# Kernel tuning notes

Hardware: AMD Instinct MI355X
Metric: run time of the kernel (lower is better)

The kernel has to match this reference:

```python
import jax, jax.numpy as jnp
import numpy as np

N, E, F_IN, H, G, C = 50000, 600000, 128, 128, 500, 10


def _lin(k, fi, fo):
    # Glorot-ish scaled init for a [fi, fo] weight
    return (jax.random.normal(k, (fi, fo), jnp.float32) / np.float32(np.sqrt(fi)))


def setup_inputs() -> dict:
    key = jax.random.key(0)
    ks = jax.random.split(key, 16)
    x = jax.random.normal(ks[0], (N, F_IN), jnp.float32)
    edge_index = jax.random.randint(ks[1], (2, E), 0, N, dtype=jnp.int32)
    batch = jnp.sort(jax.random.randint(ks[2], (N,), 0, G, dtype=jnp.int32))
    return {
        "x": x, "edge_index": edge_index, "batch": batch,
        # SAGEConv i: out = mean_aggr @ Wl + bl + x @ Wr  (PyG default: mean aggr, root weight, bias on lin_l)
        "Wl1": _lin(ks[3], F_IN, H), "bl1": jnp.zeros((H,), jnp.float32), "Wr1": _lin(ks[4], F_IN, H),
        "Wl2": _lin(ks[5], H, H),    "bl2": jnp.zeros((H,), jnp.float32), "Wr2": _lin(ks[6], H, H),
        "Wl3": _lin(ks[7], H, H),    "bl3": jnp.zeros((H,), jnp.float32), "Wr3": _lin(ks[8], H, H),
        "W4": _lin(ks[9], H, 64), "b4": jnp.zeros((64,), jnp.float32),
        "W5": _lin(ks[10], 64, C), "b5": jnp.zeros((C,), jnp.float32),
    }


def _segment_mean(vals, ids, num_segments):
    s = jax.ops.segment_sum(vals, ids, num_segments=num_segments)
    cnt = jax.ops.segment_sum(jnp.ones((vals.shape[0], 1), vals.dtype), ids, num_segments=num_segments)
    return s / jnp.maximum(cnt, 1.0)


def _sage_conv(x, src, dst, Wl, bl, Wr):
    # gather source features along edges, mean-aggregate at destinations
    aggr = _segment_mean(x[src], dst, N)  # [N, F]
    return aggr @ Wl + bl + x @ Wr


def reference(x, edge_index, batch, Wl1, bl1, Wr1, Wl2, bl2, Wr2, Wl3, bl3, Wr3, W4, b4, W5, b5):
    src, dst = edge_index[0], edge_index[1]
    h = jax.nn.relu(_sage_conv(x, src, dst, Wl1, bl1, Wr1))
    h = jax.nn.relu(_sage_conv(h, src, dst, Wl2, bl2, Wr2))
    h = jax.nn.relu(_sage_conv(h, src, dst, Wl3, bl3, Wr3))
    g = _segment_mean(h, batch, G)          # global mean pool -> [G, H]
    g = jax.nn.relu(g @ W4 + b4)
    return jax.nn.log_softmax(g @ W5 + b5, axis=-1)
```

## Files before the change

### kernel.cpp

```cpp
#include <hip/hip_runtime.h>
#include <hip/hip_bf16.h>
#include <math.h>

#define FH 128

typedef __attribute__((ext_vector_type(8))) short short8v;
typedef __attribute__((ext_vector_type(4))) float float4v;
typedef unsigned short ushort_t;
typedef unsigned int   uint32;

__device__ __forceinline__ ushort_t f2bf(float f) {
    uint32 u = __builtin_bit_cast(uint32, f);
    u += 0x7fffu + ((u >> 16) & 1u);
    return (ushort_t)(u >> 16);
}
__device__ __forceinline__ float bf_lo(uint32 w) { return __builtin_bit_cast(float, w << 16); }
__device__ __forceinline__ float bf_hi(uint32 w) { return __builtin_bit_cast(float, w & 0xffff0000u); }
__device__ __forceinline__ uint32 pack2(float lo, float hi) {
    return (uint32)f2bf(lo) | ((uint32)f2bf(hi) << 16);
}

__device__ __forceinline__ void pack_one(const float* __restrict__ Wl,
                                         const float* __restrict__ Wr,
                                         ushort_t* __restrict__ Bp, int t) {
    int k = t >> 7, n = t & 127;
    float v = (k < FH) ? Wl[k * FH + n] : Wr[(k - FH) * FH + n];
    int nt = n >> 4, kt = k >> 5;
    int lane = (n & 15) + (((k >> 3) & 3) << 4);
    int j = k & 7;
    Bp[(((nt * 8 + kt) * 64) + lane) * 8 + j] = f2bf(v);
}

__global__ __launch_bounds__(256) void prep_kernel(
        const float* __restrict__ x, ushort_t* __restrict__ xb, size_t n, int cvtBlocks,
        const float* __restrict__ Wl1, const float* __restrict__ Wr1, ushort_t* __restrict__ Bp1,
        const float* __restrict__ Wl2, const float* __restrict__ Wr2, ushort_t* __restrict__ Bp2,
        const float* __restrict__ Wl3, const float* __restrict__ Wr3, ushort_t* __restrict__ Bp3,
        int* __restrict__ deg, int N) {
    int b = blockIdx.x;
    if (b < cvtBlocks) {
        size_t base = ((size_t)b * 256 + threadIdx.x) * 8;
        if (base >= n) return;
        const float4 a = *(const float4*)(x + base);
        const float4 c = *(const float4*)(x + base + 4);
        ushort_t o[8] = {f2bf(a.x), f2bf(a.y), f2bf(a.z), f2bf(a.w),
                         f2bf(c.x), f2bf(c.y), f2bf(c.z), f2bf(c.w)};
        *(uint4*)(xb + base) = *(const uint4*)o;
        return;
    }
    b -= cvtBlocks;
    if (b < 384) {
        int which = b >> 7;
        int t = (b & 127) * 256 + threadIdx.x;
        if (which == 0)      pack_one(Wl1, Wr1, Bp1, t);
        else if (which == 1) pack_one(Wl2, Wr2, Bp2, t);
        else                 pack_one(Wl3, Wr3, Bp3, t);
        return;
    }
    b -= 384;
    {
        int i = (b * 256 + threadIdx.x) * 4;
        if (i + 3 < N) {
            *(int4*)(deg + i) = make_int4(0, 0, 0, 0);
        } else {
            for (int j = i; j < N; ++j) deg[j] = 0;
        }
    }
}

__global__ __launch_bounds__(256) void deg_kernel(const int* __restrict__ dst,
                                                  int* __restrict__ deg, int E) {
    int e = blockIdx.x * 256 + threadIdx.x;
    if (e < E) atomicAdd(&deg[dst[e]], 1);
}

__global__ __launch_bounds__(256) void scan1_kernel(const int* __restrict__ deg,
                                                    int* __restrict__ rowptr,
                                                    int* __restrict__ blockSums, int N) {
    __shared__ int lds[256];
    const int base = blockIdx.x * 1024;
    const int t = threadIdx.x;
    int v[4]; int sum = 0;
    #pragma unroll
    for (int j = 0; j < 4; ++j) {
        int idx = base + t * 4 + j;
        v[j] = (idx < N) ? deg[idx] : 0;
        sum += v[j];
    }
    lds[t] = sum; __syncthreads();
    for (int off = 1; off < 256; off <<= 1) {
        int val = lds[t];
        int add = (t >= off) ? lds[t - off] : 0;
        __syncthreads();
        lds[t] = val + add;
        __syncthreads();
    }
    int run = (t > 0) ? lds[t - 1] : 0;
    #pragma unroll
    for (int j = 0; j < 4; ++j) {
        int idx = base + t * 4 + j;
        if (idx < N) rowptr[idx] = run;
        run += v[j];
    }
    if (t == 255) blockSums[blockIdx.x] = lds[255];
}

__global__ __launch_bounds__(256) void scan3_gb_kernel(int* __restrict__ rowptr,
                                                       int* __restrict__ pos,
                                                       const int* __restrict__ blockSums,
                                                       int N, int nb,
                                                       const int* __restrict__ batch,
                                                       int* __restrict__ gstart, int G) {
    if ((int)blockIdx.x >= nb) {
        int g = ((int)blockIdx.x - nb) * 256 + threadIdx.x;
        if (g > G) return;
        int lo = 0, hi = N;
        while (lo < hi) {
            int mid = (lo + hi) >> 1;
            if (batch[mid] < g) lo = mid + 1; else hi = mid;
        }
        gstart[g] = lo;
        return;
    }
    __shared__ int sAdd, sTot;
    if (threadIdx.x < 64) {
        const int lane = threadIdx.x;
        const int bid = blockIdx.x;
        int pre = 0, tot = 0;
        for (int i = lane; i < nb; i += 64) {
            const int v = blockSums[i];
            tot += v;
            if (i < bid) pre += v;
        }
        #pragma unroll
        for (int off = 1; off < 64; off <<= 1) {
            pre += __shfl_xor(pre, off);
            tot += __shfl_xor(tot, off);
        }
        if (lane == 0) { sAdd = pre; sTot = tot; }
    }
    __syncthreads();
    const int add = sAdd;
    const int base = blockIdx.x * 1024;
    #pragma unroll
    for (int j = 0; j < 4; ++j) {
        int idx = base + threadIdx.x * 4 + j;
        if (idx < N) {
            int v = rowptr[idx] + add;
            rowptr[idx] = v;
            pos[idx] = v;
        }
    }
    if (blockIdx.x == (unsigned)(nb - 1) && threadIdx.x == 0) rowptr[N] = sTot;
}

__global__ __launch_bounds__(256) void fill_csr_kernel(const int* __restrict__ src,
                                                       const int* __restrict__ dst,
                                                       int* __restrict__ pos,
                                                       int* __restrict__ csr, int E) {
    int e = (blockIdx.x * 256 + threadIdx.x) * 2;
    if (e >= E) return;
    if (e + 1 < E) {
        const int2 s2 = *(const int2*)(src + e);
        const int2 d2 = *(const int2*)(dst + e);
        int i0 = atomicAdd(&pos[d2.x], 1);
        int i1 = atomicAdd(&pos[d2.y], 1);
        csr[i0] = s2.x;
        csr[i1] = s2.y;
    } else {
        int idx = atomicAdd(&pos[dst[e]], 1);
        csr[idx] = src[e];
    }
}

__global__ __launch_bounds__(256) void pull_mean_kernel(const ushort_t* __restrict__ x,
                                                        const int* __restrict__ rowptr,
                                                        const int* __restrict__ csr,
                                                        ushort_t* __restrict__ aggr, int N) {
    const int v = (blockIdx.x * 256 + threadIdx.x) >> 6;
    if (v >= N) return;
    const int lane = threadIdx.x & 63;
    const int grp  = lane >> 4;
    const int li   = lane & 15;
    const int beg = rowptr[v], end = rowptr[v + 1];
    const uint4* xp = (const uint4*)x + li;

    const uint4 z = {0u, 0u, 0u, 0u};
    uint4 w0 = z, w1 = z, w2 = z, w3 = z, w4 = z, w5 = z;
    const int i0 = beg + grp;
    if (i0 < end)      w0 = xp[(size_t)csr[i0] * 16];
    if (i0 + 4 < end)  w1 = xp[(size_t)csr[i0 + 4] * 16];
    if (i0 + 8 < end)  w2 = xp[(size_t)csr[i0 + 8] * 16];
    if (i0 + 12 < end) w3 = xp[(size_t)csr[i0 + 12] * 16];
    if (i0 + 16 < end) w4 = xp[(size_t)csr[i0 + 16] * 16];
    if (i0 + 20 < end) w5 = xp[(size_t)csr[i0 + 20] * 16];

    float a0 = (bf_lo(w0.x) + bf_lo(w1.x)) + (bf_lo(w2.x) + bf_lo(w3.x)) + (bf_lo(w4.x) + bf_lo(w5.x));
    float a1 = (bf_hi(w0.x) + bf_hi(w1.x)) + (bf_hi(w2.x) + bf_hi(w3.x)) + (bf_hi(w4.x) + bf_hi(w5.x));
    float a2 = (bf_lo(w0.y) + bf_lo(w1.y)) + (bf_lo(w2.y) + bf_lo(w3.y)) + (bf_lo(w4.y) + bf_lo(w5.y));
    float a3 = (bf_hi(w0.y) + bf_hi(w1.y)) + (bf_hi(w2.y) + bf_hi(w3.y)) + (bf_hi(w4.y) + bf_hi(w5.y));
    float a4 = (bf_lo(w0.z) + bf_lo(w1.z)) + (bf_lo(w2.z) + bf_lo(w3.z)) + (bf_lo(w4.z) + bf_lo(w5.z));
    float a5 = (bf_hi(w0.z) + bf_hi(w1.z)) + (bf_hi(w2.z) + bf_hi(w3.z)) + (bf_hi(w4.z) + bf_hi(w5.z));
    float a6 = (bf_lo(w0.w) + bf_lo(w1.w)) + (bf_lo(w2.w) + bf_lo(w3.w)) + (bf_lo(w4.w) + bf_lo(w5.w));
    float a7 = (bf_hi(w0.w) + bf_hi(w1.w)) + (bf_hi(w2.w) + bf_hi(w3.w)) + (bf_hi(w4.w) + bf_hi(w5.w));

    for (int i = beg + 24 + grp; i < end; i += 4) {
        const uint4 w = xp[(size_t)csr[i] * 16];
        a0 += bf_lo(w.x); a1 += bf_hi(w.x); a2 += bf_lo(w.y); a3 += bf_hi(w.y);
        a4 += bf_lo(w.z); a5 += bf_hi(w.z); a6 += bf_lo(w.w); a7 += bf_hi(w.w);
    }

    a0 += __shfl_xor(a0, 16); a1 += __shfl_xor(a1, 16);
    a2 += __shfl_xor(a2, 16); a3 += __shfl_xor(a3, 16);
    a4 += __shfl_xor(a4, 16); a5 += __shfl_xor(a5, 16);
    a6 += __shfl_xor(a6, 16); a7 += __shfl_xor(a7, 16);
    a0 += __shfl_xor(a0, 32); a1 += __shfl_xor(a1, 32);
    a2 += __shfl_xor(a2, 32); a3 += __shfl_xor(a3, 32);
    a4 += __shfl_xor(a4, 32); a5 += __shfl_xor(a5, 32);
    a6 += __shfl_xor(a6, 32); a7 += __shfl_xor(a7, 32);

    if (grp == 0) {
        const float inv = 1.0f / (float)max(end - beg, 1);
        uint4 o;
        o.x = pack2(a0 * inv, a1 * inv);
        o.y = pack2(a2 * inv, a3 * inv);
        o.z = pack2(a4 * inv, a5 * inv);
        o.w = pack2(a6 * inv, a7 * inv);
        ((uint4*)aggr)[(size_t)v * 16 + li] = o;
    }
}

#define SO_STRIDE 136
__global__ __launch_bounds__(512) void sage_mfma_kernel(const ushort_t* __restrict__ xin,
                                                        const ushort_t* __restrict__ aggr,
                                                        const ushort_t* __restrict__ Bp,
                                                        const float* __restrict__ bl,
                                                        ushort_t* __restrict__ out, int M) {
    __shared__ ushort_t sB[32768];
    const int tid = threadIdx.x;
    {
        const uint4* s = (const uint4*)Bp;
        uint4* d = (uint4*)sB;
        #pragma unroll
        for (int i = 0; i < 8; ++i)
            d[tid + 512 * i] = s[tid + 512 * i];
    }
    __syncthreads();

    const int wave = tid >> 6;
    const int lane = tid & 63;
    const int grp  = lane >> 4;
    const int li   = lane & 15;
    const int rowBase = (blockIdx.x * 8 + wave) * 16;
    const int arow = min(rowBase + li, M - 1);

    short8v afrag[8];
    #pragma unroll
    for (int kt = 0; kt < 4; ++kt)
        afrag[kt] = *(const short8v*)(aggr + (size_t)arow * FH + kt * 32 + grp * 8);
    #pragma unroll
    for (int kt = 0; kt < 4; ++kt)
        afrag[4 + kt] = *(const short8v*)(xin + (size_t)arow * FH + kt * 32 + grp * 8);

    float4v acc[8];
    #pragma unroll
    for (int nt = 0; nt < 8; ++nt) {
        acc[nt] = (float4v){0.f, 0.f, 0.f, 0.f};
        #pragma unroll
        for (int kt = 0; kt < 8; ++kt) {
            const short8v b = *(const short8v*)(sB + (((nt * 8 + kt) * 64) + lane) * 8);
            acc[nt] = __builtin_amdgcn_mfma_f32_16x16x32_bf16(afrag[kt], b, acc[nt], 0, 0, 0);
        }
    }

    __syncthreads();

    ushort_t* so = sB + wave * (16 * SO_STRIDE);
    #pragma unroll
    for (int nt = 0; nt < 8; ++nt) {
        const float bias = bl[nt * 16 + li];
        #pragma unroll
        for (int r = 0; r < 4; ++r)
            so[(grp * 4 + r) * SO_STRIDE + nt * 16 + li] = f2bf(fmaxf(acc[nt][r] + bias, 0.f));
    }
    #pragma unroll
    for (int t = 0; t < 4; ++t) {
        const int idx = lane + 64 * t;
        const int r  = idx >> 4;
        const int ch = idx & 15;
        const int row = rowBase + r;
        if (row < M) {
            const uint4 val = *(const uint4*)(so + r * SO_STRIDE + ch * 8);
            *(uint4*)(out + (size_t)row * FH + ch * 8) = val;
        }
    }
}

__global__ __launch_bounds__(256) void head_kernel(const ushort_t* __restrict__ h,
                                                   const int* __restrict__ gstart,
                                                   const float* __restrict__ W4,
                                                   const float* __restrict__ b4,
                                                   const float* __restrict__ W5,
                                                   const float* __restrict__ b5,
                                                   float* __restrict__ out, int G) {
    __shared__ float sred[4][FH];
    __shared__ float sg2[64];
    __shared__ float sl[10];
    __shared__ float slse;
    const int g = blockIdx.x;
    const int t = threadIdx.x;
    const int wave = t >> 6, lane = t & 63;
    const int beg = gstart[g], end = gstart[g + 1];

    const uint32* hp = (const uint32*)h + lane;
    float a0 = 0.f, a1 = 0.f;
    for (int i = beg + wave; i < end; i += 4) {
        const uint32 w = hp[(size_t)i * 64];
        a0 += bf_lo(w); a1 += bf_hi(w);
    }
    sred[wave][lane * 2]     = a0;
    sred[wave][lane * 2 + 1] = a1;
    __syncthreads();
    if (t < FH) {
        const float s = sred[0][t] + sred[1][t] + sred[2][t] + sred[3][t];
        sred[0][t] = s / (float)max(end - beg, 1);
    }
    __syncthreads();
    if (t < 64) {
        float acc = b4[t];
        #pragma unroll 4
        for (int k = 0; k < FH; ++k)
            acc += sred[0][k] * W4[k * 64 + t];
        sg2[t] = fmaxf(acc, 0.f);
    }
    __syncthreads();
    if (t < 10) {
        float acc = b5[t];
        #pragma unroll 4
        for (int k = 0; k < 64; ++k)
            acc += sg2[k] * W5[k * 10 + t];
        sl[t] = acc;
    }
    __syncthreads();
    if (t == 0) {
        float m = sl[0];
        #pragma unroll
        for (int j = 1; j < 10; ++j) m = fmaxf(m, sl[j]);
        float s = 0.f;
        #pragma unroll
        for (int j = 0; j < 10; ++j) s += expf(sl[j] - m);
        slse = m + logf(s);
    }
    __syncthreads();
    if (t < 10) out[g * 10 + t] = sl[t] - slse;
}

extern "C" void kernel_launch(void* const* d_in, const int* in_sizes, int n_in,
                              void* d_out, int out_size, void* d_ws, size_t ws_size,
                              hipStream_t stream) {
    const float* x     = (const float*)d_in[0];
    const int*   ei    = (const int*)d_in[1];
    const int*   batch = (const int*)d_in[2];
    const float* Wl1 = (const float*)d_in[3];
    const float* bl1 = (const float*)d_in[4];
    const float* Wr1 = (const float*)d_in[5];
    const float* Wl2 = (const float*)d_in[6];
    const float* bl2 = (const float*)d_in[7];
    const float* Wr2 = (const float*)d_in[8];
    const float* Wl3 = (const float*)d_in[9];
    const float* bl3 = (const float*)d_in[10];
    const float* Wr3 = (const float*)d_in[11];
    const float* W4  = (const float*)d_in[12];
    const float* b4  = (const float*)d_in[13];
    const float* W5  = (const float*)d_in[14];
    const float* b5  = (const float*)d_in[15];
    float* out = (float*)d_out;

    const int N = in_sizes[0] / FH;
    const int E = in_sizes[1] / 2;
    const int G = out_size / 10;
    const int* src = ei;
    const int* dst = ei + E;

    char* p = (char*)d_ws;
    auto take = [&](size_t bytes) { char* q = p; p += (bytes + 255) & ~(size_t)255; return q; };
    ushort_t* xb    = (ushort_t*)take((size_t)N * FH * 2);
    ushort_t* h     = (ushort_t*)take((size_t)N * FH * 2);
    ushort_t* aggrb = (ushort_t*)take((size_t)N * FH * 2);
    int* deg        = (int*)take((size_t)N * 4);
    int* rowptr     = (int*)take((size_t)(N + 1) * 4);
    int* pos        = (int*)take((size_t)N * 4);
    int* csr        = (int*)take((size_t)E * 4);
    int* blockSums  = (int*)take(256 * 4);
    ushort_t* Bp1   = (ushort_t*)take(256 * FH * 2);
    ushort_t* Bp2   = (ushort_t*)take(256 * FH * 2);
    ushort_t* Bp3   = (ushort_t*)take(256 * FH * 2);
    int* gstart     = (int*)take((size_t)(G + 1) * 4);

    const int nb = (N + 1023) / 1024;

    const int cvtBlocks  = (int)(((size_t)N * FH / 8 + 255) / 256);
    const int zeroBlocks = (N / 4 + 255) / 256;
    prep_kernel<<<cvtBlocks + 384 + zeroBlocks, 256, 0, stream>>>(
        x, xb, (size_t)N * FH, cvtBlocks,
        Wl1, Wr1, Bp1, Wl2, Wr2, Bp2, Wl3, Wr3, Bp3,
        deg, N);

    deg_kernel<<<(E + 255) / 256, 256, 0, stream>>>(dst, deg, E);

    const int gbBlocks = (G + 1 + 255) / 256;
    scan1_kernel<<<nb, 256, 0, stream>>>(deg, rowptr, blockSums, N);
    scan3_gb_kernel<<<nb + gbBlocks, 256, 0, stream>>>(rowptr, pos, blockSums, N, nb,
                                                       batch, gstart, G);
    fill_csr_kernel<<<(E / 2 + 255) / 256, 256, 0, stream>>>(src, dst, pos, csr, E);

    const int pullGrid = (N * 64 + 255) / 256;
    const int gemmGrid = (N + 127) / 128;

    pull_mean_kernel<<<pullGrid, 256, 0, stream>>>(xb, rowptr, csr, aggrb, N);
    sage_mfma_kernel<<<gemmGrid, 512, 0, stream>>>(xb, aggrb, Bp1, bl1, h, N);

    pull_mean_kernel<<<pullGrid, 256, 0, stream>>>(h, rowptr, csr, aggrb, N);
    sage_mfma_kernel<<<gemmGrid, 512, 0, stream>>>(h, aggrb, Bp2, bl2, h, N);

    pull_mean_kernel<<<pullGrid, 256, 0, stream>>>(h, rowptr, csr, aggrb, N);
    sage_mfma_kernel<<<gemmGrid, 512, 0, stream>>>(h, aggrb, Bp3, bl3, h, N);

    head_kernel<<<G, 256, 0, stream>>>(h, gstart, W4, b4, W5, b5, out, G);
}
```

Baseline: 210.4 us.

## Fuse two-pass scan into single-pass lookback scan and use 16 lanes per node

Merges the two CSR prefix-scan kernels into one kernel that publishes each block's sum with an agent-scope flag; later blocks spin on earlier blocks' flags to get their prefix. The flags live just past the degree array, so prep_kernel now zeroes them too. The mean-aggregation gather now gives each node 16 lanes instead of 64, with 12 neighbour loads unrolled and no cross-lane shuffle reduction. This cuts one launch and the shuffle work, at the cost of spin-waiting that assumes earlier blocks get scheduled, and less parallelism per node for high-degree nodes.

Result: slower. 227.1 us (+8.0%).

```diff
diff --git a/kernel.cpp b/kernel.cpp
--- a/kernel.cpp
+++ b/kernel.cpp
@@ -36,7 +36,7 @@
         const float* __restrict__ Wl1, const float* __restrict__ Wr1, ushort_t* __restrict__ Bp1,
         const float* __restrict__ Wl2, const float* __restrict__ Wr2, ushort_t* __restrict__ Bp2,
         const float* __restrict__ Wl3, const float* __restrict__ Wr3, ushort_t* __restrict__ Bp3,
-        int* __restrict__ deg, int N) {
+        int* __restrict__ deg, int Nz) {
     int b = blockIdx.x;
     if (b < cvtBlocks) {
         size_t base = ((size_t)b * 256 + threadIdx.x) * 8;
@@ -60,10 +60,10 @@
     b -= 384;
     {
         int i = (b * 256 + threadIdx.x) * 4;
-        if (i + 3 < N) {
+        if (i + 3 < Nz) {
             *(int4*)(deg + i) = make_int4(0, 0, 0, 0);
         } else {
-            for (int j = i; j < N; ++j) deg[j] = 0;
+            for (int j = i; j < Nz; ++j) deg[j] = 0;
         }
     }
 }
@@ -74,43 +74,14 @@
     if (e < E) atomicAdd(&deg[dst[e]], 1);
 }
 
-__global__ __launch_bounds__(256) void scan1_kernel(const int* __restrict__ deg,
-                                                    int* __restrict__ rowptr,
-                                                    int* __restrict__ blockSums, int N) {
-    __shared__ int lds[256];
-    const int base = blockIdx.x * 1024;
-    const int t = threadIdx.x;
-    int v[4]; int sum = 0;
-    #pragma unroll
-    for (int j = 0; j < 4; ++j) {
-        int idx = base + t * 4 + j;
-        v[j] = (idx < N) ? deg[idx] : 0;
-        sum += v[j];
-    }
-    lds[t] = sum; __syncthreads();
-    for (int off = 1; off < 256; off <<= 1) {
-        int val = lds[t];
-        int add = (t >= off) ? lds[t - off] : 0;
-        __syncthreads();
-        lds[t] = val + add;
-        __syncthreads();
-    }
-    int run = (t > 0) ? lds[t - 1] : 0;
-    #pragma unroll
-    for (int j = 0; j < 4; ++j) {
-        int idx = base + t * 4 + j;
-        if (idx < N) rowptr[idx] = run;
-        run += v[j];
-    }
-    if (t == 255) blockSums[blockIdx.x] = lds[255];
-}
-
-__global__ __launch_bounds__(256) void scan3_gb_kernel(int* __restrict__ rowptr,
-                                                       int* __restrict__ pos,
-                                                       const int* __restrict__ blockSums,
-                                                       int N, int nb,
-                                                       const int* __restrict__ batch,
-                                                       int* __restrict__ gstart, int G) {
+__global__ __launch_bounds__(256) void scan_lb_kernel(const int* __restrict__ deg,
+                                                      int* __restrict__ rowptr,
+                                                      int* __restrict__ pos,
+                                                      int* __restrict__ lsum,
+                                                      int* __restrict__ lflag,
+                                                      int N, int nb,
+                                                      const int* __restrict__ batch,
+                                                      int* __restrict__ gstart, int G) {
     if ((int)blockIdx.x >= nb) {
         int g = ((int)blockIdx.x - nb) * 256 + threadIdx.x;
         if (g > G) return;
@@ -122,36 +93,53 @@
         gstart[g] = lo;
         return;
     }
-    __shared__ int sAdd, sTot;
-    if (threadIdx.x < 64) {
-        const int lane = threadIdx.x;
-        const int bid = blockIdx.x;
-        int pre = 0, tot = 0;
-        for (int i = lane; i < nb; i += 64) {
-            const int v = blockSums[i];
-            tot += v;
-            if (i < bid) pre += v;
+    __shared__ int lds[256];
+    __shared__ int sPre;
+    const int b = blockIdx.x;
+    const int base = b * 1024;
+    const int t = threadIdx.x;
+    int v[4]; int sum = 0;
+    #pragma unroll
+    for (int j = 0; j < 4; ++j) {
+        int idx = base + t * 4 + j;
+        v[j] = (idx < N) ? deg[idx] : 0;
+        sum += v[j];
+    }
+    lds[t] = sum; __syncthreads();
+    for (int off = 1; off < 256; off <<= 1) {
+        int val = lds[t];
+        int add = (t >= off) ? lds[t - off] : 0;
+        __syncthreads();
+        lds[t] = val + add;
+        __syncthreads();
+    }
+    if (t == 255) {
+        __hip_atomic_store(&lsum[b], lds[255], __ATOMIC_RELAXED, __HIP_MEMORY_SCOPE_AGENT);
+        __hip_atomic_store(&lflag[b], 1, __ATOMIC_RELEASE, __HIP_MEMORY_SCOPE_AGENT);
+    }
+    if (t < 64) {
+        int pre = 0;
+        if (t < b) {
+            while (__hip_atomic_load(&lflag[t], __ATOMIC_ACQUIRE, __HIP_MEMORY_SCOPE_AGENT) == 0) {}
+            pre = __hip_atomic_load(&lsum[t], __ATOMIC_RELAXED, __HIP_MEMORY_SCOPE_AGENT);
         }
         #pragma unroll
-        for (int off = 1; off < 64; off <<= 1) {
+        for (int off = 1; off < 64; off <<= 1)
             pre += __shfl_xor(pre, off);
-            tot += __shfl_xor(tot, off);
-        }
-        if (lane == 0) { sAdd = pre; sTot = tot; }
-    }
-    __syncthreads();
-    const int add = sAdd;
-    const int base = blockIdx.x * 1024;
+        if (t == 0) sPre = pre;
+    }
+    __syncthreads();
+    const int add = sPre;
+    int run = add + ((t > 0) ? lds[t - 1] : 0) - sum;
+    int ex = add + ((t > 0) ? lds[t - 1] : 0);
+    (void)run;
     #pragma unroll
     for (int j = 0; j < 4; ++j) {
-        int idx = base + threadIdx.x * 4 + j;
-        if (idx < N) {
-            int v = rowptr[idx] + add;
-            rowptr[idx] = v;
-            pos[idx] = v;
-        }
-    }
-    if (blockIdx.x == (unsigned)(nb - 1) && threadIdx.x == 0) rowptr[N] = sTot;
+        int idx = base + t * 4 + j;
+        if (idx < N) { rowptr[idx] = ex; pos[idx] = ex; }
+        ex += v[j];
+    }
+    if (b == nb - 1 && t == 255) rowptr[N] = add + lds[255];
 }
 
 __global__ __launch_bounds__(256) void fill_csr_kernel(const int* __restrict__ src,
@@ -177,57 +165,42 @@
                                                         const int* __restrict__ rowptr,
                                                         const int* __restrict__ csr,
                                                         ushort_t* __restrict__ aggr, int N) {
-    const int v = (blockIdx.x * 256 + threadIdx.x) >> 6;
-    if (v >= N) return;
-    const int lane = threadIdx.x & 63;
-    const int grp  = lane >> 4;
-    const int li   = lane & 15;
-    const int beg = rowptr[v], end = rowptr[v + 1];
+    const int node = (blockIdx.x * 256 + threadIdx.x) >> 4;
+    if (node >= N) return;
+    const int li = threadIdx.x & 15;
+    const int beg = rowptr[node], end = rowptr[node + 1];
     const uint4* xp = (const uint4*)x + li;
 
     const uint4 z = {0u, 0u, 0u, 0u};
-    uint4 w0 = z, w1 = z, w2 = z, w3 = z, w4 = z, w5 = z;
-    const int i0 = beg + grp;
-    if (i0 < end)      w0 = xp[(size_t)csr[i0] * 16];
-    if (i0 + 4 < end)  w1 = xp[(size_t)csr[i0 + 4] * 16];
-    if (i0 + 8 < end)  w2 = xp[(size_t)csr[i0 + 8] * 16];
-    if (i0 + 12 < end) w3 = xp[(size_t)csr[i0 + 12] * 16];
-    if (i0 + 16 < end) w4 = xp[(size_t)csr[i0 + 16] * 16];
-    if (i0 + 20 < end) w5 = xp[(size_t)csr[i0 + 20] * 16];
-
-    float a0 = (bf_lo(w0.x) + bf_lo(w1.x)) + (bf_lo(w2.x) + bf_lo(w3.x)) + (bf_lo(w4.x) + bf_lo(w5.x));
-    float a1 = (bf_hi(w0.x) + bf_hi(w1.x)) + (bf_hi(w2.x) + bf_hi(w3.x)) + (bf_hi(w4.x) + bf_hi(w5.x));
-    float a2 = (bf_lo(w0.y) + bf_lo(w1.y)) + (bf_lo(w2.y) + bf_lo(w3.y)) + (bf_lo(w4.y) + bf_lo(w5.y));
-    float a3 = (bf_hi(w0.y) + bf_hi(w1.y)) + (bf_hi(w2.y) + bf_hi(w3.y)) + (bf_hi(w4.y) + bf_hi(w5.y));
-    float a4 = (bf_lo(w0.z) + bf_lo(w1.z)) + (bf_lo(w2.z) + bf_lo(w3.z)) + (bf_lo(w4.z) + bf_lo(w5.z));
-    float a5 = (bf_hi(w0.z) + bf_hi(w1.z)) + (bf_hi(w2.z) + bf_hi(w3.z)) + (bf_hi(w4.z) + bf_hi(w5.z));
-    float a6 = (bf_lo(w0.w) + bf_lo(w1.w)) + (bf_lo(w2.w) + bf_lo(w3.w)) + (bf_lo(w4.w) + bf_lo(w5.w));
-    float a7 = (bf_hi(w0.w) + bf_hi(w1.w)) + (bf_hi(w2.w) + bf_hi(w3.w)) + (bf_hi(w4.w) + bf_hi(w5.w));
-
-    for (int i = beg + 24 + grp; i < end; i += 4) {
-        const uint4 w = xp[(size_t)csr[i] * 16];
-        a0 += bf_lo(w.x); a1 += bf_hi(w.x); a2 += bf_lo(w.y); a3 += bf_hi(w.y);
-        a4 += bf_lo(w.z); a5 += bf_hi(w.z); a6 += bf_lo(w.w); a7 += bf_hi(w.w);
-    }
-
-    a0 += __shfl_xor(a0, 16); a1 += __shfl_xor(a1, 16);
-    a2 += __shfl_xor(a2, 16); a3 += __shfl_xor(a3, 16);
-    a4 += __shfl_xor(a4, 16); a5 += __shfl_xor(a5, 16);
-    a6 += __shfl_xor(a6, 16); a7 += __shfl_xor(a7, 16);
-    a0 += __shfl_xor(a0, 32); a1 += __shfl_xor(a1, 32);
-    a2 += __shfl_xor(a2, 32); a3 += __shfl_xor(a3, 32);
-    a4 += __shfl_xor(a4, 32); a5 += __shfl_xor(a5, 32);
-    a6 += __shfl_xor(a6, 32); a7 += __shfl_xor(a7, 32);
-
-    if (grp == 0) {
-        const float inv = 1.0f / (float)max(end - beg, 1);
-        uint4 o;
-        o.x = pack2(a0 * inv, a1 * inv);
-        o.y = pack2(a2 * inv, a3 * inv);
-        o.z = pack2(a4 * inv, a5 * inv);
-        o.w = pack2(a6 * inv, a7 * inv);
-        ((uint4*)aggr)[(size_t)v * 16 + li] = o;
-    }
+    uint4 w[12];
+    #pragma unroll
+    for (int k = 0; k < 12; ++k)
+        w[k] = (beg + k < end) ? xp[(size_t)csr[beg + k] * 16] : z;
+
+    float a0 = 0.f, a1 = 0.f, a2 = 0.f, a3 = 0.f;
+    float a4 = 0.f, a5 = 0.f, a6 = 0.f, a7 = 0.f;
+    #pragma unroll
+    for (int k = 0; k < 12; ++k) {
+        a0 += bf_lo(w[k].x); a1 += bf_hi(w[k].x);
+        a2 += bf_lo(w[k].y); a3 += bf_hi(w[k].y);
+        a4 += bf_lo(w[k].z); a5 += bf_hi(w[k].z);
+        a6 += bf_lo(w[k].w); a7 += bf_hi(w[k].w);
+    }
+    for (int i = beg + 12; i < end; ++i) {
+        const uint4 ww = xp[(size_t)csr[i] * 16];
+        a0 += bf_lo(ww.x); a1 += bf_hi(ww.x);
+        a2 += bf_lo(ww.y); a3 += bf_hi(ww.y);
+        a4 += bf_lo(ww.z); a5 += bf_hi(ww.z);
+        a6 += bf_lo(ww.w); a7 += bf_hi(ww.w);
+    }
+
+    const float inv = 1.0f / (float)max(end - beg, 1);
+    uint4 o;
+    o.x = pack2(a0 * inv, a1 * inv);
+    o.y = pack2(a2 * inv, a3 * inv);
+    o.z = pack2(a4 * inv, a5 * inv);
+    o.w = pack2(a6 * inv, a7 * inv);
+    ((uint4*)aggr)[(size_t)node * 16 + li] = o;
 }
 
 #define SO_STRIDE 136
@@ -387,11 +360,12 @@
     ushort_t* xb    = (ushort_t*)take((size_t)N * FH * 2);
     ushort_t* h     = (ushort_t*)take((size_t)N * FH * 2);
     ushort_t* aggrb = (ushort_t*)take((size_t)N * FH * 2);
-    int* deg        = (int*)take((size_t)N * 4);
+    int* deg        = (int*)take((size_t)(N + 64) * 4);
+    int* lflag      = deg + N;
     int* rowptr     = (int*)take((size_t)(N + 1) * 4);
     int* pos        = (int*)take((size_t)N * 4);
     int* csr        = (int*)take((size_t)E * 4);
-    int* blockSums  = (int*)take(256 * 4);
+    int* lsum       = (int*)take(256 * 4);
     ushort_t* Bp1   = (ushort_t*)take(256 * FH * 2);
     ushort_t* Bp2   = (ushort_t*)take(256 * FH * 2);
     ushort_t* Bp3   = (ushort_t*)take(256 * FH * 2);
@@ -400,21 +374,20 @@
     const int nb = (N + 1023) / 1024;
 
     const int cvtBlocks  = (int)(((size_t)N * FH / 8 + 255) / 256);
-    const int zeroBlocks = (N / 4 + 255) / 256;
+    const int zeroBlocks = ((N + 64) / 4 + 255) / 256;
     prep_kernel<<<cvtBlocks + 384 + zeroBlocks, 256, 0, stream>>>(
         x, xb, (size_t)N * FH, cvtBlocks,
         Wl1, Wr1, Bp1, Wl2, Wr2, Bp2, Wl3, Wr3, Bp3,
-        deg, N);
+        deg, N + 64);
 
     deg_kernel<<<(E + 255) / 256, 256, 0, stream>>>(dst, deg, E);
 
     const int gbBlocks = (G + 1 + 255) / 256;
-    scan1_kernel<<<nb, 256, 0, stream>>>(deg, rowptr, blockSums, N);
-    scan3_gb_kernel<<<nb + gbBlocks, 256, 0, stream>>>(rowptr, pos, blockSums, N, nb,
-                                                       batch, gstart, G);
+    scan_lb_kernel<<<nb + gbBlocks, 256, 0, stream>>>(deg, rowptr, pos, lsum, lflag,
+                                                      N, nb, batch, gstart, G);
     fill_csr_kernel<<<(E / 2 + 255) / 256, 256, 0, stream>>>(src, dst, pos, csr, E);
 
-    const int pullGrid = (N * 64 + 255) / 256;
+    const int pullGrid = (N * 16 + 255) / 256;
     const int gemmGrid = (N + 127) / 128;
 
     pull_mean_kernel<<<pullGrid, 256, 0, stream>>>(xb, rowptr, csr, aggrb, N);
```

## Fuse CSR construction stages into one cooperative kernel with grid syncs

Applied to the files above, without the earlier changes.

The separate kernels for zeroing degrees, counting degrees, block scan, scan fixup plus graph-start search, and CSR fill become one cooperative kernel of 1024 blocks that separates the phases with grid-wide syncs. Degree zeroing moves out of the prep kernel into this kernel. The aim is to remove several kernel launches and their inter-kernel gaps. In exchange, the edge phases are limited to a fixed grid using grid-stride loops, and each grid.sync adds its own cost.

Measured after the change: 572.9 us. 2.72x slower.

```diff
diff --git a/kernel.cpp b/kernel.cpp
--- a/kernel.cpp
+++ b/kernel.cpp
@@ -1,5 +1,6 @@
 #include <hip/hip_runtime.h>
 #include <hip/hip_bf16.h>
+#include <hip/hip_cooperative_groups.h>
 #include <math.h>
 
 #define FH 128
@@ -35,8 +36,7 @@
         const float* __restrict__ x, ushort_t* __restrict__ xb, size_t n, int cvtBlocks,
         const float* __restrict__ Wl1, const float* __restrict__ Wr1, ushort_t* __restrict__ Bp1,
         const float* __restrict__ Wl2, const float* __restrict__ Wr2, ushort_t* __restrict__ Bp2,
-        const float* __restrict__ Wl3, const float* __restrict__ Wr3, ushort_t* __restrict__ Bp3,
-        int* __restrict__ deg, int N) {
+        const float* __restrict__ Wl3, const float* __restrict__ Wr3, ushort_t* __restrict__ Bp3) {
     int b = blockIdx.x;
     if (b < cvtBlocks) {
         size_t base = ((size_t)b * 256 + threadIdx.x) * 8;
@@ -49,127 +49,120 @@
         return;
     }
     b -= cvtBlocks;
-    if (b < 384) {
+    {
         int which = b >> 7;
         int t = (b & 127) * 256 + threadIdx.x;
         if (which == 0)      pack_one(Wl1, Wr1, Bp1, t);
         else if (which == 1) pack_one(Wl2, Wr2, Bp2, t);
         else                 pack_one(Wl3, Wr3, Bp3, t);
-        return;
-    }
-    b -= 384;
-    {
-        int i = (b * 256 + threadIdx.x) * 4;
-        if (i + 3 < N) {
-            *(int4*)(deg + i) = make_int4(0, 0, 0, 0);
+    }
+}
+
+__global__ __launch_bounds__(256) void csr_coop_kernel(const int* __restrict__ src,
+                                                       const int* __restrict__ dst,
+                                                       int* __restrict__ deg,
+                                                       int* __restrict__ rowptr,
+                                                       int* __restrict__ pos,
+                                                       int* __restrict__ csr,
+                                                       int* __restrict__ blockSums,
+                                                       const int* __restrict__ batch,
+                                                       int* __restrict__ gstart,
+                                                       int N, int E, int G, int nb) {
+    cooperative_groups::grid_group grid = cooperative_groups::this_grid();
+    const int t   = threadIdx.x;
+    const int bid = blockIdx.x;
+    const int nthr = gridDim.x * 256;
+    const int gtid = bid * 256 + t;
+
+    for (int i = gtid; i < N; i += nthr) deg[i] = 0;
+    grid.sync();
+
+    for (int e = gtid; e < E; e += nthr) atomicAdd(&deg[dst[e]], 1);
+    grid.sync();
+
+    if (bid < nb) {
+        __shared__ int lds[256];
+        const int base = bid * 1024;
+        int v[4]; int sum = 0;
+        #pragma unroll
+        for (int j = 0; j < 4; ++j) {
+            int idx = base + t * 4 + j;
+            v[j] = (idx < N) ? deg[idx] : 0;
+            sum += v[j];
+        }
+        lds[t] = sum; __syncthreads();
+        for (int off = 1; off < 256; off <<= 1) {
+            int val = lds[t];
+            int add = (t >= off) ? lds[t - off] : 0;
+            __syncthreads();
+            lds[t] = val + add;
+            __syncthreads();
+        }
+        int run = (t > 0) ? lds[t - 1] : 0;
+        #pragma unroll
+        for (int j = 0; j < 4; ++j) {
+            int idx = base + t * 4 + j;
+            if (idx < N) rowptr[idx] = run;
+            run += v[j];
+        }
+        if (t == 255) blockSums[bid] = lds[255];
+    } else if (bid < nb + 2) {
+        int g = (bid - nb) * 256 + t;
+        if (g <= G) {
+            int lo = 0, hi = N;
+            while (lo < hi) {
+                int mid = (lo + hi) >> 1;
+                if (batch[mid] < g) lo = mid + 1; else hi = mid;
+            }
+            gstart[g] = lo;
+        }
+    }
+    grid.sync();
+
+    if (bid < nb) {
+        __shared__ int sAdd, sTot;
+        if (t < 64) {
+            int pre = 0, tot = 0;
+            for (int i = t; i < nb; i += 64) {
+                const int v = blockSums[i];
+                tot += v;
+                if (i < bid) pre += v;
+            }
+            #pragma unroll
+            for (int off = 1; off < 64; off <<= 1) {
+                pre += __shfl_xor(pre, off);
+                tot += __shfl_xor(tot, off);
+            }
+            if (t == 0) { sAdd = pre; sTot = tot; }
+        }
+        __syncthreads();
+        const int add = sAdd;
+        const int base = bid * 1024;
+        #pragma unroll
+        for (int j = 0; j < 4; ++j) {
+            int idx = base + t * 4 + j;
+            if (idx < N) {
+                int v = rowptr[idx] + add;
+                rowptr[idx] = v;
+                pos[idx] = v;
+            }
+        }
+        if (bid == nb - 1 && t == 0) rowptr[N] = sTot;
+    }
+    grid.sync();
+
+    for (int e = gtid * 2; e < E; e += nthr * 2) {
+        if (e + 1 < E) {
+            const int2 s2 = *(const int2*)(src + e);
+            const int2 d2 = *(const int2*)(dst + e);
+            int i0 = atomicAdd(&pos[d2.x], 1);
+            int i1 = atomicAdd(&pos[d2.y], 1);
+            csr[i0] = s2.x;
+            csr[i1] = s2.y;
         } else {
-            for (int j = i; j < N; ++j) deg[j] = 0;
-        }
-    }
-}
-
-__global__ __launch_bounds__(256) void deg_kernel(const int* __restrict__ dst,
-                                                  int* __restrict__ deg, int E) {
-    int e = blockIdx.x * 256 + threadIdx.x;
-    if (e < E) atomicAdd(&deg[dst[e]], 1);
-}
-
-__global__ __launch_bounds__(256) void scan1_kernel(const int* __restrict__ deg,
-                                                    int* __restrict__ rowptr,
-                                                    int* __restrict__ blockSums, int N) {
-    __shared__ int lds[256];
-    const int base = blockIdx.x * 1024;
-    const int t = threadIdx.x;
-    int v[4]; int sum = 0;
-    #pragma unroll
-    for (int j = 0; j < 4; ++j) {
-        int idx = base + t * 4 + j;
-        v[j] = (idx < N) ? deg[idx] : 0;
-        sum += v[j];
-    }
-    lds[t] = sum; __syncthreads();
-    for (int off = 1; off < 256; off <<= 1) {
-        int val = lds[t];
-        int add = (t >= off) ? lds[t - off] : 0;
-        __syncthreads();
-        lds[t] = val + add;
-        __syncthreads();
-    }
-    int run = (t > 0) ? lds[t - 1] : 0;
-    #pragma unroll
-    for (int j = 0; j < 4; ++j) {
-        int idx = base + t * 4 + j;
-        if (idx < N) rowptr[idx] = run;
-        run += v[j];
-    }
-    if (t == 255) blockSums[blockIdx.x] = lds[255];
-}
-
-__global__ __launch_bounds__(256) void scan3_gb_kernel(int* __restrict__ rowptr,
-                                                       int* __restrict__ pos,
-                                                       const int* __restrict__ blockSums,
-                                                       int N, int nb,
-                                                       const int* __restrict__ batch,
-                                                       int* __restrict__ gstart, int G) {
-    if ((int)blockIdx.x >= nb) {
-        int g = ((int)blockIdx.x - nb) * 256 + threadIdx.x;
-        if (g > G) return;
-        int lo = 0, hi = N;
-        while (lo < hi) {
-            int mid = (lo + hi) >> 1;
-            if (batch[mid] < g) lo = mid + 1; else hi = mid;
-        }
-        gstart[g] = lo;
-        return;
-    }
-    __shared__ int sAdd, sTot;
-    if (threadIdx.x < 64) {
-        const int lane = threadIdx.x;
-        const int bid = blockIdx.x;
-        int pre = 0, tot = 0;
-        for (int i = lane; i < nb; i += 64) {
-            const int v = blockSums[i];
-            tot += v;
-            if (i < bid) pre += v;
-        }
-        #pragma unroll
-        for (int off = 1; off < 64; off <<= 1) {
-            pre += __shfl_xor(pre, off);
-            tot += __shfl_xor(tot, off);
-        }
-        if (lane == 0) { sAdd = pre; sTot = tot; }
-    }
-    __syncthreads();
-    const int add = sAdd;
-    const int base = blockIdx.x * 1024;
-    #pragma unroll
-    for (int j = 0; j < 4; ++j) {
-        int idx = base + threadIdx.x * 4 + j;
-        if (idx < N) {
-            int v = rowptr[idx] + add;
-            rowptr[idx] = v;
-            pos[idx] = v;
-        }
-    }
-    if (blockIdx.x == (unsigned)(nb - 1) && threadIdx.x == 0) rowptr[N] = sTot;
-}
-
-__global__ __launch_bounds__(256) void fill_csr_kernel(const int* __restrict__ src,
-                                                       const int* __restrict__ dst,
-                                                       int* __restrict__ pos,
-                                                       int* __restrict__ csr, int E) {
-    int e = (blockIdx.x * 256 + threadIdx.x) * 2;
-    if (e >= E) return;
-    if (e + 1 < E) {
-        const int2 s2 = *(const int2*)(src + e);
-        const int2 d2 = *(const int2*)(dst + e);
-        int i0 = atomicAdd(&pos[d2.x], 1);
-        int i1 = atomicAdd(&pos[d2.y], 1);
-        csr[i0] = s2.x;
-        csr[i1] = s2.y;
-    } else {
-        int idx = atomicAdd(&pos[dst[e]], 1);
-        csr[idx] = src[e];
+            int idx = atomicAdd(&pos[dst[e]], 1);
+            csr[idx] = src[e];
+        }
     }
 }
 
@@ -397,22 +390,23 @@
     ushort_t* Bp3   = (ushort_t*)take(256 * FH * 2);
     int* gstart     = (int*)take((size_t)(G + 1) * 4);
 
-    const int nb = (N + 1023) / 1024;
-
-    const int cvtBlocks  = (int)(((size_t)N * FH / 8 + 255) / 256);
-    const int zeroBlocks = (N / 4 + 255) / 256;
-    prep_kernel<<<cvtBlocks + 384 + zeroBlocks, 256, 0, stream>>>(
+    int nb = (N + 1023) / 1024;
+
+    const int cvtBlocks = (int)(((size_t)N * FH / 8 + 255) / 256);
+    prep_kernel<<<cvtBlocks + 384, 256, 0, stream>>>(
         x, xb, (size_t)N * FH, cvtBlocks,
-        Wl1, Wr1, Bp1, Wl2, Wr2, Bp2, Wl3, Wr3, Bp3,
-        deg, N);
-
-    deg_kernel<<<(E + 255) / 256, 256, 0, stream>>>(dst, deg, E);
-
-    const int gbBlocks = (G + 1 + 255) / 256;
-    scan1_kernel<<<nb, 256, 0, stream>>>(deg, rowptr, blockSums, N);
-    scan3_gb_kernel<<<nb + gbBlocks, 256, 0, stream>>>(rowptr, pos, blockSums, N, nb,
-                                                       batch, gstart, G);
-    fill_csr_kernel<<<(E / 2 + 255) / 256, 256, 0, stream>>>(src, dst, pos, csr, E);
+        Wl1, Wr1, Bp1, Wl2, Wr2, Bp2, Wl3, Wr3, Bp3);
+
+    {
+        int N_ = N, E_ = E, G_ = G, nb_ = nb;
+        const int* src_ = src; const int* dst_ = dst;
+        int* deg_ = deg; int* rowptr_ = rowptr; int* pos_ = pos; int* csr_ = csr;
+        int* bsum_ = blockSums; const int* batch_ = batch; int* gstart_ = gstart;
+        void* args[] = {&src_, &dst_, &deg_, &rowptr_, &pos_, &csr_, &bsum_,
+                        &batch_, &gstart_, &N_, &E_, &G_, &nb_};
+        hipLaunchCooperativeKernel((const void*)csr_coop_kernel,
+                                   dim3(1024), dim3(256), args, 0, stream);
+    }
 
     const int pullGrid = (N * 64 + 255) / 256;
     const int gemmGrid = (N + 127) / 128;
```
